# Kernel tuning notes

Hardware: AMD Instinct MI355X
Metric: run time of the kernel (lower is better)

## Reference

```python
import jax, jax.numpy as jnp
import numpy as np

BN_EPS = 1e-5

def _pair_indices(f0, f1):
    row, col = [], []
    for i in range(f0):
        for j in range(i + 1, f1):
            row.append(i); col.append(j)
    return np.asarray(row, np.int32), np.asarray(col, np.int32)

def setup_inputs() -> dict:
    key = jax.random.key(0)
    ks = jax.random.split(key, 6)
    B, F0, F1, E = 4096, 32, 32, 32
    I = F0 * (F0 - 1) // 2  # 496 pairs for F0 == F1
    xi = jax.random.normal(ks[0], (B, F0, E), jnp.float32)
    xj = jax.random.normal(ks[1], (B, F1, E), jnp.float32)
    # xavier_uniform over (1, I, E): bound = sqrt(6/(I+E)) approximated by normal scale
    W = jax.random.normal(ks[2], (1, I, E), jnp.float32) * np.sqrt(2.0 / (I + E))
    bn_gamma = jnp.ones((I,), jnp.float32)
    bn_beta = jnp.zeros((I,), jnp.float32)
    attn_w = jax.random.normal(ks[3], (E, E), jnp.float32) / np.sqrt(E)
    attn_b = jnp.zeros((E,), jnp.float32)
    proj_w = jax.random.normal(ks[4], (E, 1), jnp.float32) / np.sqrt(E)
    proj_b = jnp.zeros((1,), jnp.float32)
    return {"xi": xi, "xj": xj, "W": W, "bn_gamma": bn_gamma, "bn_beta": bn_beta,
            "attn_w": attn_w, "attn_b": attn_b, "proj_w": proj_w, "proj_b": proj_b}

def reference(xi, xj, W, bn_gamma, bn_beta, attn_w, attn_b, proj_w, proj_b):
    f0, f1 = xi.shape[1], xj.shape[1]
    row, col = _pair_indices(f0, f1)
    p = xi[:, row, :]              # [B, I, E]
    q = xj[:, col, :]              # [B, I, E]
    out = p * q
    # BatchNorm1d(I) on [B, I, E] in training mode: stats over (batch, emb)
    mean = jnp.mean(out, axis=(0, 2), keepdims=True)
    var = jnp.mean(jnp.square(out - mean), axis=(0, 2), keepdims=True)
    out = (out - mean) * jax.lax.rsqrt(var + BN_EPS)
    out = out * bn_gamma[None, :, None] + bn_beta[None, :, None]
    out = out * W                   # broadcast [1, I, E]
    # attention: linear -> relu -> linear -> softmax over interaction dim
    h = jax.nn.relu(jnp.einsum('bie,ea->bia', out, attn_w) + attn_b)
    logits = jnp.einsum('bia,ao->bio', h, proj_w) + proj_b  # [B, I, 1]
    scores = jax.nn.softmax(logits, axis=1)
    return scores * out
```

## Files before the change

kernel.cpp:

```cpp
#include <hip/hip_runtime.h>

#define NB 4096
#define NF 32
#define NE 32
#define NI 496
#define BN_EPS 1e-5f
#define XPAD 36

#define SA_BLOCKS 512
#define SA_BPB    8
#define SA_CHUNK  4

typedef float f32x4_t __attribute__((ext_vector_type(4)));
typedef short bf16x8_t __attribute__((ext_vector_type(8)));

static __device__ __forceinline__ unsigned short f2bf(float f) {
    unsigned u = __builtin_bit_cast(unsigned, f);
    u = (u + 0x7FFFu + ((u >> 16) & 1u)) >> 16;
    return (unsigned short)u;
}

__device__ __forceinline__ void pair_rc_fast(int i, int& r, int& c) {
    int rr = (int)((63.0f - sqrtf(3969.0f - 8.0f * (float)i)) * 0.5f);
    int off = rr * (63 - rr) / 2;
    if (off > i) { --rr; off = rr * (63 - rr) / 2; }
    else {
        int off2 = (rr + 1) * (62 - rr) / 2;
        if (off2 <= i) { rr = rr + 1; off = off2; }
    }
    r = rr; c = rr + 1 + (i - off);
}

__global__ __launch_bounds__(256) void statsA(
        const float* __restrict__ xi, const float* __restrict__ xj,
        float* __restrict__ part) {
    __shared__ __attribute__((aligned(16))) float xi_l[SA_CHUNK * NF * XPAD];
    __shared__ __attribute__((aligned(16))) float xj_l[SA_CHUNK * NF * XPAD];
    const int t  = threadIdx.x;
    const int r  = t >> 3;
    const int cg = t & 7;

    float4 acc1[4] = {{0,0,0,0},{0,0,0,0},{0,0,0,0},{0,0,0,0}};
    float4 acc2[4] = {{0,0,0,0},{0,0,0,0},{0,0,0,0},{0,0,0,0}};

    for (int ch = 0; ch < SA_BPB / SA_CHUNK; ++ch) {
        const int b0 = blockIdx.x * SA_BPB + ch * SA_CHUNK;
        const float4* xs = (const float4*)(xi + (size_t)b0 * NF * NE);
        const float4* ys = (const float4*)(xj + (size_t)b0 * NF * NE);
        if (ch) __syncthreads();
        #pragma unroll
        for (int k = 0; k < 4; ++k) {
            const int idx = t + 256 * k;
            const int row = idx >> 3;
            const int e4  = idx & 7;
            *(float4*)&xi_l[row * XPAD + e4 * 4] = xs[idx];
            *(float4*)&xj_l[row * XPAD + e4 * 4] = ys[idx];
        }
        __syncthreads();
        #pragma unroll
        for (int bb = 0; bb < SA_CHUNK; ++bb) {
            const float* xr  = &xi_l[(bb * NF + r) * XPAD];
            const float* xc0 = &xj_l[(bb * NF) * XPAD];
            #pragma unroll
            for (int e4 = 0; e4 < 8; ++e4) {
                const float4 av = *(const float4*)&xr[e4 * 4];
                #pragma unroll
                for (int k = 0; k < 4; ++k) {
                    const int c = cg + 8 * k;
                    const float4 qv = *(const float4*)&xc0[c * XPAD + e4 * 4];
                    float px = av.x * qv.x, py = av.y * qv.y;
                    float pz = av.z * qv.z, pw = av.w * qv.w;
                    acc1[k].x += px; acc1[k].y += py;
                    acc1[k].z += pz; acc1[k].w += pw;
                    acc2[k].x += px * px; acc2[k].y += py * py;
                    acc2[k].z += pz * pz; acc2[k].w += pw * pw;
                }
            }
        }
    }

    float* dst = part + (size_t)blockIdx.x * 2048;
    #pragma unroll
    for (int k = 0; k < 4; ++k) {
        const int c = cg + 8 * k;
        const int j = r * 32 + c;
        float g1 = (acc1[k].x + acc1[k].y) + (acc1[k].z + acc1[k].w);
        float g2 = (acc2[k].x + acc2[k].y) + (acc2[k].z + acc2[k].w);
        *(float2*)&dst[2 * j] = make_float2(g1, g2);
    }
}

__global__ __launch_bounds__(256) void statsB(
        const float* __restrict__ part,
        const float* __restrict__ gamma, const float* __restrict__ beta,
        float* __restrict__ scale, float* __restrict__ shift) {
    __shared__ float red[256];
    const int t   = threadIdx.x;
    const int col = blockIdx.x * 64 + (t & 63);
    const int q   = t >> 6;
    float s = 0.f;
    #pragma unroll 8
    for (int p = q * 128; p < (q + 1) * 128; ++p)
        s += part[(size_t)p * 2048 + col];
    red[t] = s;
    __syncthreads();
    if (t < 64) red[t] = red[t] + red[t + 64] + red[t + 128] + red[t + 192];
    __syncthreads();
    if (t < 32) {
        const int cell = blockIdx.x * 32 + t;
        const int r = cell >> 5, c = cell & 31;
        if (c > r) {
            const float g1 = red[2 * t];
            const float g2 = red[2 * t + 1];
            const float invN = 1.0f / (float)(NB * NE);
            const float mean = g1 * invN;
            const float var  = g2 * invN - mean * mean;
            const int   i    = r * (63 - r) / 2 + (c - r - 1);
            const float sc   = gamma[i] / sqrtf(var + BN_EPS);
            scale[i] = sc;
            shift[i] = beta[i] - mean * sc;
        }
    }
}

__global__ __launch_bounds__(256, 4) void main_kernel(
        const float* __restrict__ xi, const float* __restrict__ xj,
        const float* __restrict__ W,
        const float* __restrict__ attn_w, const float* __restrict__ attn_b,
        const float* __restrict__ proj_w, const float* __restrict__ proj_b,
        const float* __restrict__ scale, const float* __restrict__ shift,
        float* __restrict__ out) {
    __shared__ __attribute__((aligned(16))) float xi_l[NF * XPAD];
    __shared__ __attribute__((aligned(16))) float xj_l[NF * XPAD];
    __shared__ float ss_l[NI * 2];
    __shared__ float lg[NI];
    __shared__ int   rc_l[NI];
    __shared__ float redm[4], reds[4];

    const int b    = blockIdx.x;
    const int t    = threadIdx.x;
    const int lane = t & 63;
    const int wv   = t >> 6;
    const int kc   = (lane >> 4) * 8;

    {
        const float4* x4 = (const float4*)(xi + (size_t)b * NF * NE);
        const float4* y4 = (const float4*)(xj + (size_t)b * NF * NE);
        const int r  = t >> 3;
        const int e0 = (t & 7) * 4;
        *(float4*)&xi_l[r * XPAD + e0] = x4[t];
        *(float4*)&xj_l[r * XPAD + e0] = y4[t];
        for (int s = t; s < NI; s += 256) {
            ss_l[2*s]   = scale[s];
            ss_l[2*s+1] = shift[s];
            int rr, cc; pair_rc_fast(s, rr, cc);
            rc_l[s] = (rr << 5) | cc;
        }
    }

    bf16x8_t bfr0, bfr1;
    {
        const int n = lane & 15;
        #pragma unroll
        for (int j = 0; j < 8; ++j) {
            bfr0[j] = (short)f2bf(attn_w[(kc + j) * NE + n]);
            bfr1[j] = (short)f2bf(attn_w[(kc + j) * NE + n + 16]);
        }
    }
    const float abn0 = attn_b[lane & 15];
    const float abn1 = attn_b[(lane & 15) + 16];
    const float pwn0 = proj_w[lane & 15];
    const float pwn1 = proj_w[(lane & 15) + 16];
    const float pb   = proj_b[0];
    __syncthreads();

    float o_reg[8][8];
    #pragma unroll
    for (int mt = 0; mt < 8; ++mt) {
        const int m = wv + 4 * mt;
        if (m < 31) {
            const int i  = m * 16 + (lane & 15);
            const int rc = rc_l[i];
            const int r  = rc >> 5, c = rc & 31;
            const float sc = ss_l[2*i], sh = ss_l[2*i+1];
            const float4 a0 = *(const float4*)&xi_l[r * XPAD + kc];
            const float4 a1 = *(const float4*)&xi_l[r * XPAD + kc + 4];
            const float4 q0 = *(const float4*)&xj_l[c * XPAD + kc];
            const float4 q1 = *(const float4*)&xj_l[c * XPAD + kc + 4];
            const float4 w0 = *(const float4*)&W[i * NE + kc];
            const float4 w1 = *(const float4*)&W[i * NE + kc + 4];
            o_reg[mt][0] = w0.x * (sc * a0.x * q0.x + sh);
            o_reg[mt][1] = w0.y * (sc * a0.y * q0.y + sh);
            o_reg[mt][2] = w0.z * (sc * a0.z * q0.z + sh);
            o_reg[mt][3] = w0.w * (sc * a0.w * q0.w + sh);
            o_reg[mt][4] = w1.x * (sc * a1.x * q1.x + sh);
            o_reg[mt][5] = w1.y * (sc * a1.y * q1.y + sh);
            o_reg[mt][6] = w1.z * (sc * a1.z * q1.z + sh);
            o_reg[mt][7] = w1.w * (sc * a1.w * q1.w + sh);

            bf16x8_t af;
            #pragma unroll
            for (int j = 0; j < 8; ++j) af[j] = (short)f2bf(o_reg[mt][j]);

            f32x4_t c0 = {0.f, 0.f, 0.f, 0.f};
            f32x4_t c1 = {0.f, 0.f, 0.f, 0.f};
            c0 = __builtin_amdgcn_mfma_f32_16x16x32_bf16(af, bfr0, c0, 0, 0, 0);
            c1 = __builtin_amdgcn_mfma_f32_16x16x32_bf16(af, bfr1, c1, 0, 0, 0);
            #pragma unroll
            for (int j = 0; j < 4; ++j) {
                float v = fmaxf(c0[j] + abn0, 0.f) * pwn0
                        + fmaxf(c1[j] + abn1, 0.f) * pwn1;
                v += __shfl_xor(v, 1);
                v += __shfl_xor(v, 2);
                v += __shfl_xor(v, 4);
                v += __shfl_xor(v, 8);
                if ((lane & 15) == 0)
                    lg[m * 16 + (lane >> 4) * 4 + j] = v + pb;
            }
        }
    }
    __syncthreads();

    float m = -1e30f;
    for (int f = t; f < NI; f += 256) m = fmaxf(m, lg[f]);
    for (int off = 32; off; off >>= 1) m = fmaxf(m, __shfl_xor(m, off));
    if ((t & 63) == 0) redm[wv] = m;
    __syncthreads();
    m = fmaxf(fmaxf(redm[0], redm[1]), fmaxf(redm[2], redm[3]));

    float s = 0.f;
    for (int f = t; f < NI; f += 256) {
        const float e = expf(lg[f] - m);
        lg[f] = e;
        s += e;
    }
    for (int off = 32; off; off >>= 1) s += __shfl_xor(s, off);
    if ((t & 63) == 0) reds[wv] = s;
    __syncthreads();
    const float inv = 1.0f / ((reds[0] + reds[1]) + (reds[2] + reds[3]));

    float* outb = out + (size_t)b * NI * NE;
    #pragma unroll
    for (int mt = 0; mt < 8; ++mt) {
        const int m2 = wv + 4 * mt;
        if (m2 < 31) {
            const int i = m2 * 16 + (lane & 15);
            const float score = lg[i] * inv;
            float4 r0, r1;
            r0.x = o_reg[mt][0] * score;
            r0.y = o_reg[mt][1] * score;
            r0.z = o_reg[mt][2] * score;
            r0.w = o_reg[mt][3] * score;
            r1.x = o_reg[mt][4] * score;
            r1.y = o_reg[mt][5] * score;
            r1.z = o_reg[mt][6] * score;
            r1.w = o_reg[mt][7] * score;
            float* base = outb + i * NE + kc;
            *(float4*)base       = r0;
            *(float4*)(base + 4) = r1;
        }
    }
}

extern "C" void kernel_launch(void* const* d_in, const int* in_sizes, int n_in,
                              void* d_out, int out_size, void* d_ws, size_t ws_size,
                              hipStream_t stream) {
    const float* xi     = (const float*)d_in[0];
    const float* xj     = (const float*)d_in[1];
    const float* W      = (const float*)d_in[2];
    const float* gamma  = (const float*)d_in[3];
    const float* beta   = (const float*)d_in[4];
    const float* attn_w = (const float*)d_in[5];
    const float* attn_b = (const float*)d_in[6];
    const float* proj_w = (const float*)d_in[7];
    const float* proj_b = (const float*)d_in[8];
    float* out = (float*)d_out;

    float* part  = (float*)d_ws;
    float* scale = part + (size_t)SA_BLOCKS * 2048;
    float* shift = scale + 512;

    statsA<<<SA_BLOCKS, 256, 0, stream>>>(xi, xj, part);
    statsB<<<32, 256, 0, stream>>>(part, gamma, beta, scale, shift);
    main_kernel<<<NB, 256, 0, stream>>>(xi, xj, W, attn_w, attn_b,
                                        proj_w, proj_b, scale, shift, out);
}
```

Measured before the change: 123.7 us.

## Fold BN scale/shift into W, recompute outputs, swap MFMA operands

A new prep kernel folds the batch-norm scale and shift into W as W*scale and W*shift and precomputes the pair index table, so the main kernel needs one FMA per element. The main kernel no longer keeps the 64-float o_reg array across the softmax. It recomputes the products in the output pass to cut register pressure, drops the occupancy hint from the launch bounds, and uses the hardware packed bf16 convert. MFMA operands are swapped so the attention bias goes into the accumulator input and the projection reduces with two shuffles. statsA uses four times as many smaller blocks, adding partial-sum traffic for statsB plus an extra kernel launch.

```diff
diff --git a/kernel.cpp b/kernel.cpp
--- a/kernel.cpp
+++ b/kernel.cpp
@@ -7,17 +7,18 @@
 #define BN_EPS 1e-5f
 #define XPAD 36
 
-#define SA_BLOCKS 512
-#define SA_BPB    8
-#define SA_CHUNK  4
+#define SA_BLOCKS 2048
+#define SA_BPB    2
+#define SA_CHUNK  2
 
 typedef float f32x4_t __attribute__((ext_vector_type(4)));
 typedef short bf16x8_t __attribute__((ext_vector_type(8)));
-
-static __device__ __forceinline__ unsigned short f2bf(float f) {
-    unsigned u = __builtin_bit_cast(unsigned, f);
-    u = (u + 0x7FFFu + ((u >> 16) & 1u)) >> 16;
-    return (unsigned short)u;
+typedef unsigned u32x4_t __attribute__((ext_vector_type(4)));
+
+static __device__ __forceinline__ unsigned cvt_pk_bf16(float lo, float hi) {
+    unsigned r;
+    asm("v_cvt_pk_bf16_f32 %0, %1, %2" : "=v"(r) : "v"(lo), "v"(hi));
+    return r;
 }
 
 __device__ __forceinline__ void pair_rc_fast(int i, int& r, int& c) {
@@ -43,38 +44,35 @@
     float4 acc1[4] = {{0,0,0,0},{0,0,0,0},{0,0,0,0},{0,0,0,0}};
     float4 acc2[4] = {{0,0,0,0},{0,0,0,0},{0,0,0,0},{0,0,0,0}};
 
-    for (int ch = 0; ch < SA_BPB / SA_CHUNK; ++ch) {
-        const int b0 = blockIdx.x * SA_BPB + ch * SA_CHUNK;
-        const float4* xs = (const float4*)(xi + (size_t)b0 * NF * NE);
-        const float4* ys = (const float4*)(xj + (size_t)b0 * NF * NE);
-        if (ch) __syncthreads();
+    const int b0 = blockIdx.x * SA_BPB;
+    const float4* xs = (const float4*)(xi + (size_t)b0 * NF * NE);
+    const float4* ys = (const float4*)(xj + (size_t)b0 * NF * NE);
+    #pragma unroll
+    for (int k = 0; k < SA_CHUNK * NF * 8 / 256; ++k) {
+        const int idx = t + 256 * k;
+        const int row = idx >> 3;
+        const int e4  = idx & 7;
+        *(float4*)&xi_l[row * XPAD + e4 * 4] = xs[idx];
+        *(float4*)&xj_l[row * XPAD + e4 * 4] = ys[idx];
+    }
+    __syncthreads();
+    #pragma unroll
+    for (int bb = 0; bb < SA_CHUNK; ++bb) {
+        const float* xr  = &xi_l[(bb * NF + r) * XPAD];
+        const float* xc0 = &xj_l[(bb * NF) * XPAD];
         #pragma unroll
-        for (int k = 0; k < 4; ++k) {
-            const int idx = t + 256 * k;
-            const int row = idx >> 3;
-            const int e4  = idx & 7;
-            *(float4*)&xi_l[row * XPAD + e4 * 4] = xs[idx];
-            *(float4*)&xj_l[row * XPAD + e4 * 4] = ys[idx];
-        }
-        __syncthreads();
-        #pragma unroll
-        for (int bb = 0; bb < SA_CHUNK; ++bb) {
-            const float* xr  = &xi_l[(bb * NF + r) * XPAD];
-            const float* xc0 = &xj_l[(bb * NF) * XPAD];
+        for (int e4 = 0; e4 < 8; ++e4) {
+            const float4 av = *(const float4*)&xr[e4 * 4];
             #pragma unroll
-            for (int e4 = 0; e4 < 8; ++e4) {
-                const float4 av = *(const float4*)&xr[e4 * 4];
-                #pragma unroll
-                for (int k = 0; k < 4; ++k) {
-                    const int c = cg + 8 * k;
-                    const float4 qv = *(const float4*)&xc0[c * XPAD + e4 * 4];
-                    float px = av.x * qv.x, py = av.y * qv.y;
-                    float pz = av.z * qv.z, pw = av.w * qv.w;
-                    acc1[k].x += px; acc1[k].y += py;
-                    acc1[k].z += pz; acc1[k].w += pw;
-                    acc2[k].x += px * px; acc2[k].y += py * py;
-                    acc2[k].z += pz * pz; acc2[k].w += pw * pw;
-                }
+            for (int k = 0; k < 4; ++k) {
+                const int c = cg + 8 * k;
+                const float4 qv = *(const float4*)&xc0[c * XPAD + e4 * 4];
+                float px = av.x * qv.x, py = av.y * qv.y;
+                float pz = av.z * qv.z, pw = av.w * qv.w;
+                acc1[k].x += px; acc1[k].y += py;
+                acc1[k].z += pz; acc1[k].w += pw;
+                acc2[k].x += px * px; acc2[k].y += py * py;
+                acc2[k].z += pz * pz; acc2[k].w += pw * pw;
             }
         }
     }
@@ -100,7 +98,7 @@
     const int q   = t >> 6;
     float s = 0.f;
     #pragma unroll 8
-    for (int p = q * 128; p < (q + 1) * 128; ++p)
+    for (int p = q * (SA_BLOCKS/4); p < (q + 1) * (SA_BLOCKS/4); ++p)
         s += part[(size_t)p * 2048 + col];
     red[t] = s;
     __syncthreads();
@@ -123,16 +121,32 @@
     }
 }
 
-__global__ __launch_bounds__(256, 4) void main_kernel(
+__global__ __launch_bounds__(256) void prep_kernel(
+        const float* __restrict__ W,
+        const float* __restrict__ scale, const float* __restrict__ shift,
+        float* __restrict__ W2, float* __restrict__ Wsh, int* __restrict__ rc_tab) {
+    const int idx = blockIdx.x * 256 + threadIdx.x;
+    if (idx < NI * NE) {
+        const int i = idx >> 5;
+        const float w = W[idx];
+        W2[idx]  = w * scale[i];
+        Wsh[idx] = w * shift[i];
+    }
+    if (idx < NI) {
+        int r, c; pair_rc_fast(idx, r, c);
+        rc_tab[idx] = (r << 5) | c;
+    }
+}
+
+__global__ __launch_bounds__(256) void main_kernel(
         const float* __restrict__ xi, const float* __restrict__ xj,
-        const float* __restrict__ W,
+        const float* __restrict__ W2, const float* __restrict__ Wsh,
         const float* __restrict__ attn_w, const float* __restrict__ attn_b,
         const float* __restrict__ proj_w, const float* __restrict__ proj_b,
-        const float* __restrict__ scale, const float* __restrict__ shift,
+        const int* __restrict__ rc_tab,
         float* __restrict__ out) {
     __shared__ __attribute__((aligned(16))) float xi_l[NF * XPAD];
     __shared__ __attribute__((aligned(16))) float xj_l[NF * XPAD];
-    __shared__ float ss_l[NI * 2];
     __shared__ float lg[NI];
     __shared__ int   rc_l[NI];
     __shared__ float redm[4], reds[4];
@@ -142,6 +156,8 @@
     const int lane = t & 63;
     const int wv   = t >> 6;
     const int kc   = (lane >> 4) * 8;
+    const int lr   = lane & 15;
+    const int ar   = (lane >> 4) * 4;
 
     {
         const float4* x4 = (const float4*)(xi + (size_t)b * NF * NE);
@@ -150,111 +166,125 @@
         const int e0 = (t & 7) * 4;
         *(float4*)&xi_l[r * XPAD + e0] = x4[t];
         *(float4*)&xj_l[r * XPAD + e0] = y4[t];
-        for (int s = t; s < NI; s += 256) {
-            ss_l[2*s]   = scale[s];
-            ss_l[2*s+1] = shift[s];
-            int rr, cc; pair_rc_fast(s, rr, cc);
-            rc_l[s] = (rr << 5) | cc;
-        }
-    }
-
-    bf16x8_t bfr0, bfr1;
+        for (int s = t; s < NI; s += 256) rc_l[s] = rc_tab[s];
+    }
+
+    bf16x8_t awf0, awf1;
     {
-        const int n = lane & 15;
+        u32x4_t p0, p1;
         #pragma unroll
-        for (int j = 0; j < 8; ++j) {
-            bfr0[j] = (short)f2bf(attn_w[(kc + j) * NE + n]);
-            bfr1[j] = (short)f2bf(attn_w[(kc + j) * NE + n + 16]);
-        }
-    }
-    const float abn0 = attn_b[lane & 15];
-    const float abn1 = attn_b[(lane & 15) + 16];
-    const float pwn0 = proj_w[lane & 15];
-    const float pwn1 = proj_w[(lane & 15) + 16];
-    const float pb   = proj_b[0];
-    __syncthreads();
-
-    float o_reg[8][8];
+        for (int q = 0; q < 4; ++q) {
+            p0[q] = cvt_pk_bf16(attn_w[(kc + 2*q)     * NE + lr],
+                                attn_w[(kc + 2*q + 1) * NE + lr]);
+            p1[q] = cvt_pk_bf16(attn_w[(kc + 2*q)     * NE + lr + 16],
+                                attn_w[(kc + 2*q + 1) * NE + lr + 16]);
+        }
+        awf0 = __builtin_bit_cast(bf16x8_t, p0);
+        awf1 = __builtin_bit_cast(bf16x8_t, p1);
+    }
+    f32x4_t cin0, cin1;
+    float pwj0[4], pwj1[4];
+    #pragma unroll
+    for (int j = 0; j < 4; ++j) {
+        cin0[j] = attn_b[ar + j];
+        cin1[j] = attn_b[ar + j + 16];
+        pwj0[j] = proj_w[ar + j];
+        pwj1[j] = proj_w[ar + j + 16];
+    }
+    const float pb = proj_b[0];
+    __syncthreads();
+
     #pragma unroll
     for (int mt = 0; mt < 8; ++mt) {
         const int m = wv + 4 * mt;
         if (m < 31) {
-            const int i  = m * 16 + (lane & 15);
+            const int i  = m * 16 + lr;
             const int rc = rc_l[i];
             const int r  = rc >> 5, c = rc & 31;
-            const float sc = ss_l[2*i], sh = ss_l[2*i+1];
             const float4 a0 = *(const float4*)&xi_l[r * XPAD + kc];
             const float4 a1 = *(const float4*)&xi_l[r * XPAD + kc + 4];
             const float4 q0 = *(const float4*)&xj_l[c * XPAD + kc];
             const float4 q1 = *(const float4*)&xj_l[c * XPAD + kc + 4];
-            const float4 w0 = *(const float4*)&W[i * NE + kc];
-            const float4 w1 = *(const float4*)&W[i * NE + kc + 4];
-            o_reg[mt][0] = w0.x * (sc * a0.x * q0.x + sh);
-            o_reg[mt][1] = w0.y * (sc * a0.y * q0.y + sh);
-            o_reg[mt][2] = w0.z * (sc * a0.z * q0.z + sh);
-            o_reg[mt][3] = w0.w * (sc * a0.w * q0.w + sh);
-            o_reg[mt][4] = w1.x * (sc * a1.x * q1.x + sh);
-            o_reg[mt][5] = w1.y * (sc * a1.y * q1.y + sh);
-            o_reg[mt][6] = w1.z * (sc * a1.z * q1.z + sh);
-            o_reg[mt][7] = w1.w * (sc * a1.w * q1.w + sh);
-
-            bf16x8_t af;
-            #pragma unroll
-            for (int j = 0; j < 8; ++j) af[j] = (short)f2bf(o_reg[mt][j]);
-
-            f32x4_t c0 = {0.f, 0.f, 0.f, 0.f};
-            f32x4_t c1 = {0.f, 0.f, 0.f, 0.f};
-            c0 = __builtin_amdgcn_mfma_f32_16x16x32_bf16(af, bfr0, c0, 0, 0, 0);
-            c1 = __builtin_amdgcn_mfma_f32_16x16x32_bf16(af, bfr1, c1, 0, 0, 0);
+            const float4 w20 = *(const float4*)&W2[i * NE + kc];
+            const float4 w21 = *(const float4*)&W2[i * NE + kc + 4];
+            const float4 s0  = *(const float4*)&Wsh[i * NE + kc];
+            const float4 s1  = *(const float4*)&Wsh[i * NE + kc + 4];
+            float o0 = fmaf(w20.x, a0.x * q0.x, s0.x);
+            float o1 = fmaf(w20.y, a0.y * q0.y, s0.y);
+            float o2 = fmaf(w20.z, a0.z * q0.z, s0.z);
+            float o3 = fmaf(w20.w, a0.w * q0.w, s0.w);
+            float o4 = fmaf(w21.x, a1.x * q1.x, s1.x);
+            float o5 = fmaf(w21.y, a1.y * q1.y, s1.y);
+            float o6 = fmaf(w21.z, a1.z * q1.z, s1.z);
+            float o7 = fmaf(w21.w, a1.w * q1.w, s1.w);
+            u32x4_t pk;
+            pk[0] = cvt_pk_bf16(o0, o1);
+            pk[1] = cvt_pk_bf16(o2, o3);
+            pk[2] = cvt_pk_bf16(o4, o5);
+            pk[3] = cvt_pk_bf16(o6, o7);
+            const bf16x8_t of = __builtin_bit_cast(bf16x8_t, pk);
+
+            f32x4_t c0 = __builtin_amdgcn_mfma_f32_16x16x32_bf16(awf0, of, cin0, 0, 0, 0);
+            f32x4_t c1 = __builtin_amdgcn_mfma_f32_16x16x32_bf16(awf1, of, cin1, 0, 0, 0);
+
+            float v = 0.f;
             #pragma unroll
             for (int j = 0; j < 4; ++j) {
-                float v = fmaxf(c0[j] + abn0, 0.f) * pwn0
-                        + fmaxf(c1[j] + abn1, 0.f) * pwn1;
-                v += __shfl_xor(v, 1);
-                v += __shfl_xor(v, 2);
-                v += __shfl_xor(v, 4);
-                v += __shfl_xor(v, 8);
-                if ((lane & 15) == 0)
-                    lg[m * 16 + (lane >> 4) * 4 + j] = v + pb;
+                v = fmaf(fmaxf(c0[j], 0.f), pwj0[j], v);
+                v = fmaf(fmaxf(c1[j], 0.f), pwj1[j], v);
             }
-        }
-    }
-    __syncthreads();
-
-    float m = -1e30f;
-    for (int f = t; f < NI; f += 256) m = fmaxf(m, lg[f]);
-    for (int off = 32; off; off >>= 1) m = fmaxf(m, __shfl_xor(m, off));
-    if ((t & 63) == 0) redm[wv] = m;
-    __syncthreads();
-    m = fmaxf(fmaxf(redm[0], redm[1]), fmaxf(redm[2], redm[3]));
-
-    float s = 0.f;
+            v += __shfl_xor(v, 16);
+            v += __shfl_xor(v, 32);
+            if (lr == lane) ;
+            if (lane < 16) lg[m * 16 + lane] = v + pb;
+        }
+    }
+    __syncthreads();
+
+    float mx = -1e30f;
+    for (int f = t; f < NI; f += 256) mx = fmaxf(mx, lg[f]);
+    for (int off = 32; off; off >>= 1) mx = fmaxf(mx, __shfl_xor(mx, off));
+    if ((t & 63) == 0) redm[wv] = mx;
+    __syncthreads();
+    mx = fmaxf(fmaxf(redm[0], redm[1]), fmaxf(redm[2], redm[3]));
+
+    float sm = 0.f;
     for (int f = t; f < NI; f += 256) {
-        const float e = expf(lg[f] - m);
+        const float e = __expf(lg[f] - mx);
         lg[f] = e;
-        s += e;
-    }
-    for (int off = 32; off; off >>= 1) s += __shfl_xor(s, off);
-    if ((t & 63) == 0) reds[wv] = s;
+        sm += e;
+    }
+    for (int off = 32; off; off >>= 1) sm += __shfl_xor(sm, off);
+    if ((t & 63) == 0) reds[wv] = sm;
     __syncthreads();
     const float inv = 1.0f / ((reds[0] + reds[1]) + (reds[2] + reds[3]));
 
     float* outb = out + (size_t)b * NI * NE;
     #pragma unroll
     for (int mt = 0; mt < 8; ++mt) {
-        const int m2 = wv + 4 * mt;
-        if (m2 < 31) {
-            const int i = m2 * 16 + (lane & 15);
+        const int m = wv + 4 * mt;
+        if (m < 31) {
+            const int i  = m * 16 + lr;
+            const int rc = rc_l[i];
+            const int r  = rc >> 5, c = rc & 31;
             const float score = lg[i] * inv;
+            const float4 a0 = *(const float4*)&xi_l[r * XPAD + kc];
+            const float4 a1 = *(const float4*)&xi_l[r * XPAD + kc + 4];
+            const float4 q0 = *(const float4*)&xj_l[c * XPAD + kc];
+            const float4 q1 = *(const float4*)&xj_l[c * XPAD + kc + 4];
+            const float4 w20 = *(const float4*)&W2[i * NE + kc];
+            const float4 w21 = *(const float4*)&W2[i * NE + kc + 4];
+            const float4 s0  = *(const float4*)&Wsh[i * NE + kc];
+            const float4 s1  = *(const float4*)&Wsh[i * NE + kc + 4];
             float4 r0, r1;
-            r0.x = o_reg[mt][0] * score;
-            r0.y = o_reg[mt][1] * score;
-            r0.z = o_reg[mt][2] * score;
-            r0.w = o_reg[mt][3] * score;
-            r1.x = o_reg[mt][4] * score;
-            r1.y = o_reg[mt][5] * score;
-            r1.z = o_reg[mt][6] * score;
-            r1.w = o_reg[mt][7] * score;
+            r0.x = score * fmaf(w20.x, a0.x * q0.x, s0.x);
+            r0.y = score * fmaf(w20.y, a0.y * q0.y, s0.y);
+            r0.z = score * fmaf(w20.z, a0.z * q0.z, s0.z);
+            r0.w = score * fmaf(w20.w, a0.w * q0.w, s0.w);
+            r1.x = score * fmaf(w21.x, a1.x * q1.x, s1.x);
+            r1.y = score * fmaf(w21.y, a1.y * q1.y, s1.y);
+            r1.z = score * fmaf(w21.z, a1.z * q1.z, s1.z);
+            r1.w = score * fmaf(w21.w, a1.w * q1.w, s1.w);
             float* base = outb + i * NE + kc;
             *(float4*)base       = r0;
             *(float4*)(base + 4) = r1;
@@ -276,12 +306,16 @@
     const float* proj_b = (const float*)d_in[8];
     float* out = (float*)d_out;
 
-    float* part  = (float*)d_ws;
-    float* scale = part + (size_t)SA_BLOCKS * 2048;
-    float* shift = scale + 512;
+    float* part   = (float*)d_ws;
+    float* scale  = part + (size_t)SA_BLOCKS * 2048;
+    float* shift  = scale + 512;
+    float* W2     = shift + 512;
+    float* Wsh    = W2 + NI * NE;
+    int*   rc_tab = (int*)(Wsh + NI * NE);
 
     statsA<<<SA_BLOCKS, 256, 0, stream>>>(xi, xj, part);
     statsB<<<32, 256, 0, stream>>>(part, gamma, beta, scale, shift);
-    main_kernel<<<NB, 256, 0, stream>>>(xi, xj, W, attn_w, attn_b,
-                                        proj_w, proj_b, scale, shift, out);
-}
+    prep_kernel<<<62, 256, 0, stream>>>(W, scale, shift, W2, Wsh, rc_tab);
+    main_kernel<<<NB, 256, 0, stream>>>(xi, xj, W2, Wsh, attn_w, attn_b,
+                                        proj_w, proj_b, rc_tab, out);
+}
```

Measured after the change: 219.3 us. 1.77x slower.
